# Kernel tuning notes

Hardware: AMD Instinct MI355X
Metric: run time of the kernel (lower is better)

The kernel has to match this reference:

```python
import jax, jax.numpy as jnp
import numpy as np

N_NODES = 100000
N_EDGES = 1600000
D = 128


def _graph_conv(x, src, dst, norm_src, norm_dst, W, b):
    # DGL GraphConv, norm='both': out = D_dst^{-1/2} A D_src^{-1/2} x W + b
    xs = x * norm_src[:, None]                 # [N, d] scale by src (out-)degree
    agg = jax.ops.segment_sum(xs[src], dst, num_segments=N_NODES)  # SpMM
    hd = agg * norm_dst[:, None]
    return hd @ W + b


def setup_inputs() -> dict:
    key = jax.random.key(0)
    ks = jax.random.split(key, 9)
    h = jax.random.normal(ks[0], (N_NODES, D), dtype=jnp.float32)
    src = jax.random.randint(ks[1], (N_EDGES,), 0, N_NODES, dtype=jnp.int64)
    dst = jax.random.randint(ks[2], (N_EDGES,), 0, N_NODES, dtype=jnp.int64)
    s = 1.0 / np.sqrt(D)
    W0 = jax.random.uniform(ks[3], (D, D), jnp.float32, -s, s)
    b0 = jnp.zeros((D,), jnp.float32)
    W1 = jax.random.uniform(ks[4], (D, D), jnp.float32, -s, s)
    b1 = jnp.zeros((D,), jnp.float32)
    W2 = jax.random.uniform(ks[5], (D, D), jnp.float32, -s, s)
    b2 = jnp.zeros((D,), jnp.float32)
    return {"h": h, "src": src, "dst": dst, "W0": W0, "b0": b0,
            "W1": W1, "b1": b1, "W2": W2, "b2": b2}


def reference(h, src, dst, W0, b0, W1, b1, W2, b2):
    ones = jnp.ones((N_EDGES,), jnp.float32)
    deg_out = jnp.maximum(jax.ops.segment_sum(ones, src, num_segments=N_NODES), 1.0)
    deg_in = jnp.maximum(jax.ops.segment_sum(ones, dst, num_segments=N_NODES), 1.0)
    norm_src = deg_out ** -0.5
    norm_dst = deg_in ** -0.5

    x = jax.nn.relu(_graph_conv(h, src, dst, norm_src, norm_dst, W0, b0))
    x = jax.nn.relu(_graph_conv(x, src, dst, norm_src, norm_dst, W1, b1))
    x = _graph_conv(x, src, dst, norm_src, norm_dst, W2, b2)
    # dgl.mean_nodes over a single graph -> [1, out_size]
    return jnp.mean(x, axis=0, keepdims=True)
```

## Files before the change

kernel.cpp:

```cpp
#include <hip/hip_runtime.h>
#include <hip/hip_fp16.h>

#define N_NODES 100000
#define N_EDGES 1600000
#define D 128
#define BKT_SHIFT 9
#define BKT_N 512
#define NBKT 196
#define CAP 10240
#define NBLK_B 512
#define EPB (N_EDGES / NBLK_B)
#define ZUINT4 ((2 * N_NODES + 128) / 4)

typedef _Float16 f16x4 __attribute__((ext_vector_type(4)));
typedef _Float16 f16x8 __attribute__((ext_vector_type(8)));
typedef float f32x4 __attribute__((ext_vector_type(4)));
typedef float f32x2 __attribute__((ext_vector_type(2)));

__global__ __launch_bounds__(256) void
k_zwt(const float* __restrict__ W0, const float* __restrict__ W1,
      __half* __restrict__ Wt, uint4* __restrict__ zbase,
      unsigned int* __restrict__ gcur) {
    if (blockIdx.x < 128) {
        int i = blockIdx.x * 256 + threadIdx.x;
        int l = i >> 14, r = i & (D * D - 1);
        int n = r >> 7, k = r & 127;
        const float* W = l ? W1 : W0;
        Wt[i] = __float2half(W[k * D + n]);
        return;
    }
    if (blockIdx.x == 128 && threadIdx.x < NBKT)
        gcur[threadIdx.x] = (unsigned)threadIdx.x * CAP;
    int i = (blockIdx.x - 128) * 256 + threadIdx.x;
    if (i < ZUINT4) zbase[i] = (uint4){0u, 0u, 0u, 0u};
}

__global__ __launch_bounds__(256) void
k_bucket(const int* __restrict__ src, const int* __restrict__ dst,
         unsigned int* __restrict__ gcur, unsigned int* __restrict__ packed,
         int* __restrict__ cnt_src) {
    __shared__ int hist[NBKT];
    __shared__ unsigned int base[NBKT];
    __shared__ int cur[NBKT];
    int tid = threadIdx.x;
    for (int i = tid; i < NBKT; i += 256) hist[i] = 0;
    __syncthreads();
    int e0 = blockIdx.x * EPB;
    for (int i = e0 + tid; i < e0 + EPB; i += 256)
        atomicAdd(&hist[dst[i] >> BKT_SHIFT], 1);
    __syncthreads();
    for (int i = tid; i < NBKT; i += 256) {
        base[i] = atomicAdd(&gcur[i], (unsigned)hist[i]);
        cur[i] = 0;
    }
    __syncthreads();
    for (int i = e0 + tid; i < e0 + EPB; i += 256) {
        int d = dst[i], s = src[i];
        int b = d >> BKT_SHIFT;
        int off = atomicAdd(&cur[b], 1);
        unsigned int pos = base[b] + (unsigned)off;
        if (pos < (unsigned)(b + 1) * CAP)
            packed[pos] = ((unsigned)(d & (BKT_N - 1)) << 17) | (unsigned)s;
        atomicAdd(&cnt_src[s], 1);
    }
}

__global__ __launch_bounds__(256) void
k_cscan(const unsigned int* __restrict__ gcur, int* __restrict__ cbase,
        int* __restrict__ rpD) {
    __shared__ int sc[2][256];
    int tid = threadIdx.x;
    int m = (tid < NBKT) ? (int)(gcur[tid] - (unsigned)tid * CAP) : 0;
    sc[0][tid] = m;
    int pb = 0;
    for (int d = 1; d < 256; d <<= 1) {
        __syncthreads();
        int v = sc[pb][tid];
        if (tid >= d) v += sc[pb][tid - d];
        sc[pb ^ 1][tid] = v;
        pb ^= 1;
    }
    __syncthreads();
    cbase[tid] = tid ? sc[pb][tid - 1] : 0;
    if (tid == 255) { cbase[256] = sc[pb][255]; rpD[N_NODES] = sc[pb][255]; }
}

__global__ __launch_bounds__(256) void
k_csr(const unsigned int* __restrict__ gcur, const int* __restrict__ cbase,
      const unsigned int* __restrict__ packed, int* __restrict__ csr_src,
      int* __restrict__ rpD, float* __restrict__ nd) {
    __shared__ int cnt[BKT_N];
    __shared__ int sc[2][BKT_N];
    __shared__ int outb[CAP];
    int tid = threadIdx.x;
    int b = blockIdx.x;
    int m = (int)(gcur[b] - (unsigned)b * CAP);
    if (m > CAP) m = CAP;
    int base_in = b * CAP;
    int base_out = cbase[b];
    int n0 = b * BKT_N;
    for (int j = tid; j < BKT_N; j += 256) cnt[j] = 0;
    __syncthreads();
    for (int i = tid; i < m; i += 256)
        atomicAdd(&cnt[packed[base_in + i] >> 17], 1);
    __syncthreads();
    for (int j = tid; j < BKT_N; j += 256) sc[0][j] = cnt[j];
    int pb = 0;
    for (int d = 1; d < BKT_N; d <<= 1) {
        __syncthreads();
        for (int j = tid; j < BKT_N; j += 256) {
            int v = sc[pb][j];
            if (j >= d) v += sc[pb][j - d];
            sc[pb ^ 1][j] = v;
        }
        pb ^= 1;
    }
    __syncthreads();
    for (int j = tid; j < BKT_N; j += 256) {
        int excl = j ? sc[pb][j - 1] : 0;
        int n = n0 + j;
        if (n < N_NODES) {
            rpD[n] = base_out + excl;
            nd[n] = rsqrtf((float)max(cnt[j], 1));
        }
    }
    __syncthreads();
    for (int j = tid; j < BKT_N; j += 256)
        cnt[j] = j ? sc[pb][j - 1] : 0;
    __syncthreads();
    for (int i = tid; i < m; i += 256) {
        unsigned int p = packed[base_in + i];
        int din = p >> 17;
        int off = atomicAdd(&cnt[din], 1);
        outb[off] = (int)(p & 0x1FFFFu);
    }
    __syncthreads();
    for (int i = tid; i < m; i += 256)
        csr_src[base_out + i] = outb[i];
}

__global__ void k_prep(const float* __restrict__ x, const int* __restrict__ cnt_src,
                       unsigned int* __restrict__ out) {
    int i = blockIdx.x * 256 + threadIdx.x;
    if (i >= N_NODES * (D / 4)) return;
    int n = i >> 5;
    float4 v = ((const float4*)x)[i];
    float s = rsqrtf((float)max(cnt_src[n], 1));
    int u = __builtin_amdgcn_cvt_pk_fp8_f32(v.x * s, v.y * s, 0, false);
    u = __builtin_amdgcn_cvt_pk_fp8_f32(v.z * s, v.w * s, u, true);
    out[i] = (unsigned int)u;
}

__global__ __launch_bounds__(256) void
k_spmm(const unsigned char* __restrict__ x8, const int* __restrict__ row_ptr,
       const int* __restrict__ csr_src, __half* __restrict__ agg,
       const float* __restrict__ nd, float* __restrict__ wsum) {
    int wave = (blockIdx.x * blockDim.x + threadIdx.x) >> 6;
    int lane = threadIdx.x & 63;
    int hf = lane >> 5, l32 = lane & 31;
    if (wave >= N_NODES) return;
    int beg = row_ptr[wave], end = row_ptr[wave + 1];
    float ndr = wsum ? nd[wave] : 0.0f;
    float a0 = 0.f, a1 = 0.f, a2 = 0.f, a3 = 0.f;
    int j = beg;
    for (; j + 7 < end; j += 8) {
#pragma unroll
        for (int p = 0; p < 4; p++) {
            int s0 = csr_src[j + 2 * p];
            int s1 = csr_src[j + 2 * p + 1];
            int s = hf ? s1 : s0;
            unsigned int u = *(const unsigned int*)(x8 + (size_t)s * D + 4 * l32);
            f32x2 lo = __builtin_amdgcn_cvt_pk_f32_fp8(u, false);
            f32x2 hi = __builtin_amdgcn_cvt_pk_f32_fp8(u, true);
            a0 += lo[0]; a1 += lo[1]; a2 += hi[0]; a3 += hi[1];
            if (wsum && l32 == 0) unsafeAtomicAdd(&wsum[s], ndr);
        }
    }
    for (; j + 1 < end; j += 2) {
        int s0 = csr_src[j], s1 = csr_src[j + 1];
        int s = hf ? s1 : s0;
        unsigned int u = *(const unsigned int*)(x8 + (size_t)s * D + 4 * l32);
        f32x2 lo = __builtin_amdgcn_cvt_pk_f32_fp8(u, false);
        f32x2 hi = __builtin_amdgcn_cvt_pk_f32_fp8(u, true);
        a0 += lo[0]; a1 += lo[1]; a2 += hi[0]; a3 += hi[1];
        if (wsum && l32 == 0) unsafeAtomicAdd(&wsum[s], ndr);
    }
    if (j < end && hf == 0) {
        int s = csr_src[j];
        unsigned int u = *(const unsigned int*)(x8 + (size_t)s * D + 4 * l32);
        f32x2 lo = __builtin_amdgcn_cvt_pk_f32_fp8(u, false);
        f32x2 hi = __builtin_amdgcn_cvt_pk_f32_fp8(u, true);
        a0 += lo[0]; a1 += lo[1]; a2 += hi[0]; a3 += hi[1];
        if (wsum && l32 == 0) unsafeAtomicAdd(&wsum[s], ndr);
    }
    a0 += __shfl_xor(a0, 32, 64);
    a1 += __shfl_xor(a1, 32, 64);
    a2 += __shfl_xor(a2, 32, 64);
    a3 += __shfl_xor(a3, 32, 64);
    if (hf == 0) {
        f16x4 o;
        o[0] = (_Float16)a0; o[1] = (_Float16)a1; o[2] = (_Float16)a2; o[3] = (_Float16)a3;
        ((f16x4*)(agg + (size_t)wave * D))[l32] = o;
    }
}

__global__ __launch_bounds__(256) void
k_gemm_mfma(const __half* __restrict__ A, const __half* __restrict__ Wt,
            const float* __restrict__ b, const float* __restrict__ nd,
            const int* __restrict__ cnt_src, unsigned char* __restrict__ out) {
    int w = threadIdx.x >> 6, lane = threadIdx.x & 63;
    int m = lane & 15, q = lane >> 4;
    int row0 = blockIdx.x * 128 + w * 32;

    f16x8 zf;
#pragma unroll
    for (int j = 0; j < 8; j++) zf[j] = (_Float16)0;
    f16x8 af[2][4];
#pragma unroll
    for (int g = 0; g < 2; g++) {
        int arow = row0 + g * 16 + m;
        const f16x8* pa = (const f16x8*)(A + (size_t)arow * D);
        bool aok = arow < N_NODES;
#pragma unroll
        for (int ks = 0; ks < 4; ks++) af[g][ks] = aok ? pa[ks * 4 + q] : zf;
    }

    const f16x8* pb = (const f16x8*)Wt;
    f32x4 acc[2][8];
#pragma unroll
    for (int g = 0; g < 2; g++)
#pragma unroll
        for (int nt = 0; nt < 8; nt++) acc[g][nt] = (f32x4){0.f, 0.f, 0.f, 0.f};

#pragma unroll
    for (int ks = 0; ks < 4; ks++) {
#pragma unroll
        for (int nt = 0; nt < 8; nt++) {
            f16x8 bf = pb[((nt * 16 + m) << 4) + (ks << 2) + q];
            acc[0][nt] = __builtin_amdgcn_mfma_f32_16x16x32_f16(af[0][ks], bf, acc[0][nt], 0, 0, 0);
            acc[1][nt] = __builtin_amdgcn_mfma_f32_16x16x32_f16(af[1][ks], bf, acc[1][nt], 0, 0, 0);
        }
    }

#pragma unroll
    for (int g = 0; g < 2; g++) {
        int er = row0 + g * 16 + q * 4;
        float sd[4], ss[4];
#pragma unroll
        for (int r = 0; r < 4; r++) {
            int n = er + r;
            bool ok = n < N_NODES;
            sd[r] = ok ? nd[n] : 0.0f;
            ss[r] = ok ? rsqrtf((float)max(cnt_src[n], 1)) : 0.0f;
        }
#pragma unroll
        for (int nt = 0; nt < 8; nt++) {
            int col = nt * 16 + m;
            float bc = b[col];
#pragma unroll
            for (int r = 0; r < 4; r++) {
                int n = er + r;
                if (n < N_NODES) {
                    float v = fmaxf(sd[r] * acc[g][nt][r] + bc, 0.0f) * ss[r];
                    int pk = __builtin_amdgcn_cvt_pk_fp8_f32(v, v, 0, false);
                    out[(size_t)n * D + col] = (unsigned char)(pk & 0xff);
                }
            }
        }
    }
}

__global__ __launch_bounds__(256) void
k_gemm_red(const __half* __restrict__ A, const __half* __restrict__ Wt,
           const float* __restrict__ b, const float* __restrict__ nd,
           const int* __restrict__ cnt_src, const float* __restrict__ wsum,
           float* __restrict__ colsum) {
    __shared__ float red[128];
    int tid = threadIdx.x;
    if (tid < 128) red[tid] = 0.0f;
    __syncthreads();

    int w = tid >> 6, lane = tid & 63;
    int m = lane & 15, q = lane >> 4;
    int row0 = blockIdx.x * 128 + w * 32;

    f16x8 zf;
#pragma unroll
    for (int j = 0; j < 8; j++) zf[j] = (_Float16)0;
    f16x8 af[2][4];
#pragma unroll
    for (int g = 0; g < 2; g++) {
        int arow = row0 + g * 16 + m;
        const f16x8* pa = (const f16x8*)(A + (size_t)arow * D);
        bool aok = arow < N_NODES;
#pragma unroll
        for (int ks = 0; ks < 4; ks++) af[g][ks] = aok ? pa[ks * 4 + q] : zf;
    }

    const f16x8* pb = (const f16x8*)Wt;
    f32x4 acc[2][8];
#pragma unroll
    for (int g = 0; g < 2; g++)
#pragma unroll
        for (int nt = 0; nt < 8; nt++) acc[g][nt] = (f32x4){0.f, 0.f, 0.f, 0.f};

#pragma unroll
    for (int ks = 0; ks < 4; ks++) {
#pragma unroll
        for (int nt = 0; nt < 8; nt++) {
            f16x8 bf = pb[((nt * 16 + m) << 4) + (ks << 2) + q];
            acc[0][nt] = __builtin_amdgcn_mfma_f32_16x16x32_f16(af[0][ks], bf, acc[0][nt], 0, 0, 0);
            acc[1][nt] = __builtin_amdgcn_mfma_f32_16x16x32_f16(af[1][ks], bf, acc[1][nt], 0, 0, 0);
        }
    }

    float sd[2][4], sw[2][4];
#pragma unroll
    for (int g = 0; g < 2; g++) {
        int er = row0 + g * 16 + q * 4;
#pragma unroll
        for (int r = 0; r < 4; r++) {
            int n = er + r;
            bool ok = n < N_NODES;
            sd[g][r] = ok ? nd[n] : 0.0f;
            sw[g][r] = ok ? wsum[n] * rsqrtf((float)max(cnt_src[n], 1)) : 0.0f;
        }
    }
#pragma unroll
    for (int nt = 0; nt < 8; nt++) {
        int col = nt * 16 + m;
        float bc = b[col];
        float pc = 0.0f;
#pragma unroll
        for (int g = 0; g < 2; g++)
#pragma unroll
            for (int r = 0; r < 4; r++)
                pc += sw[g][r] * fmaxf(sd[g][r] * acc[g][nt][r] + bc, 0.0f);
        atomicAdd(&red[col], pc);
    }
    __syncthreads();
    if (tid < 128) unsafeAtomicAdd(&colsum[tid], red[tid]);
}

__global__ void k_final(const float* __restrict__ colsum, const float* __restrict__ W,
                        const float* __restrict__ b, float* __restrict__ out) {
    __shared__ float m[128];
    int j = threadIdx.x;
    m[j] = colsum[j] * (1.0f / N_NODES);
    __syncthreads();
    float acc = b[j];
    for (int k = 0; k < 128; k++)
        acc = fmaf(m[k], W[(size_t)k * D + j], acc);
    out[j] = acc;
}

extern "C" void kernel_launch(void* const* d_in, const int* in_sizes, int n_in,
                              void* d_out, int out_size, void* d_ws, size_t ws_size,
                              hipStream_t stream) {
    const float* h   = (const float*)d_in[0];
    const int*   src = (const int*)d_in[1];
    const int*   dst = (const int*)d_in[2];
    const float* W0  = (const float*)d_in[3];
    const float* b0  = (const float*)d_in[4];
    const float* W1  = (const float*)d_in[5];
    const float* b1  = (const float*)d_in[6];
    const float* W2  = (const float*)d_in[7];
    const float* b2  = (const float*)d_in[8];
    float* out = (float*)d_out;

    int*           cnt_src = (int*)d_ws;
    float*         wsum    = (float*)(cnt_src + N_NODES);
    float*         colsum  = wsum + N_NODES;
    float*         nd      = colsum + 128;
    int*           rpD     = (int*)(nd + N_NODES);
    unsigned int*  gcur    = (unsigned int*)(rpD + N_NODES + 4);
    int*           cbase   = (int*)(gcur + 256);
    __half*        Wt16    = (__half*)(cbase + 260);
    int*           csr_src = (int*)(Wt16 + 2 * D * D);
    unsigned int*  packed  = (unsigned int*)(csr_src + N_EDGES);
    unsigned char* x8      = (unsigned char*)packed;
    __half*        agg16   = (__half*)(x8 + (size_t)N_NODES * D);

    k_zwt<<<128 + (ZUINT4 + 255) / 256, 256, 0, stream>>>(
        W0, W1, Wt16, (uint4*)d_ws, gcur);
    k_bucket<<<NBLK_B, 256, 0, stream>>>(src, dst, gcur, packed, cnt_src);
    k_cscan<<<1, 256, 0, stream>>>(gcur, cbase, rpD);
    k_csr<<<NBKT, 256, 0, stream>>>(gcur, cbase, packed, csr_src, rpD, nd);

    k_prep<<<(N_NODES * (D / 4) + 255) / 256, 256, 0, stream>>>(h, cnt_src,
                                                                (unsigned int*)x8);

    k_spmm<<<(N_NODES + 3) / 4, 256, 0, stream>>>(x8, rpD, csr_src, agg16,
                                                  nd, (float*)nullptr);
    k_gemm_mfma<<<(N_NODES + 127) / 128, 256, 0, stream>>>(agg16, Wt16, b0, nd,
                                                           cnt_src, x8);
    k_spmm<<<(N_NODES + 3) / 4, 256, 0, stream>>>(x8, rpD, csr_src, agg16,
                                                  nd, wsum);
    k_gemm_red<<<(N_NODES + 127) / 128, 256, 0, stream>>>(agg16, Wt16 + (size_t)D * D,
                                                          b1, nd, cnt_src, wsum, colsum);
    k_final<<<1, 128, 0, stream>>>(colsum, W2, b2, out);
}
```

Before: 467.4 us.

## Split SpMM feature dimension into column stripes across separate blocks

```diff
diff --git a/kernel.cpp b/kernel.cpp
--- a/kernel.cpp
+++ b/kernel.cpp
@@ -11,6 +11,8 @@
 #define NBLK_B 512
 #define EPB (N_EDGES / NBLK_B)
 #define ZUINT4 ((2 * N_NODES + 128) / 4)
+#define NSTRIPE 4
+#define NBW ((N_NODES + 3) / 4)
 
 typedef _Float16 f16x4 __attribute__((ext_vector_type(4)));
 typedef _Float16 f16x8 __attribute__((ext_vector_type(8)));
@@ -155,52 +157,39 @@
 k_spmm(const unsigned char* __restrict__ x8, const int* __restrict__ row_ptr,
        const int* __restrict__ csr_src, __half* __restrict__ agg,
        const float* __restrict__ nd, float* __restrict__ wsum) {
-    int wave = (blockIdx.x * blockDim.x + threadIdx.x) >> 6;
+    int stripe = blockIdx.x / NBW;
+    int bin = blockIdx.x % NBW;
+    int wave = bin * 4 + (threadIdx.x >> 6);
     int lane = threadIdx.x & 63;
-    int hf = lane >> 5, l32 = lane & 31;
     if (wave >= N_NODES) return;
+    int eo = lane >> 3;
+    int c4 = lane & 7;
     int beg = row_ptr[wave], end = row_ptr[wave + 1];
-    float ndr = wsum ? nd[wave] : 0.0f;
+    const unsigned char* xs = x8 + stripe * 32 + 4 * c4;
+    bool do_w = (wsum != nullptr) && (stripe == 0);
+    float ndr = do_w ? nd[wave] : 0.0f;
     float a0 = 0.f, a1 = 0.f, a2 = 0.f, a3 = 0.f;
-    int j = beg;
-    for (; j + 7 < end; j += 8) {
-#pragma unroll
-        for (int p = 0; p < 4; p++) {
-            int s0 = csr_src[j + 2 * p];
-            int s1 = csr_src[j + 2 * p + 1];
-            int s = hf ? s1 : s0;
-            unsigned int u = *(const unsigned int*)(x8 + (size_t)s * D + 4 * l32);
+    for (int j = beg; j < end; j += 8) {
+        int idx = j + eo;
+        if (idx < end) {
+            int s = csr_src[idx];
+            unsigned int u = *(const unsigned int*)(xs + (size_t)s * D);
             f32x2 lo = __builtin_amdgcn_cvt_pk_f32_fp8(u, false);
             f32x2 hi = __builtin_amdgcn_cvt_pk_f32_fp8(u, true);
             a0 += lo[0]; a1 += lo[1]; a2 += hi[0]; a3 += hi[1];
-            if (wsum && l32 == 0) unsafeAtomicAdd(&wsum[s], ndr);
-        }
-    }
-    for (; j + 1 < end; j += 2) {
-        int s0 = csr_src[j], s1 = csr_src[j + 1];
-        int s = hf ? s1 : s0;
-        unsigned int u = *(const unsigned int*)(x8 + (size_t)s * D + 4 * l32);
-        f32x2 lo = __builtin_amdgcn_cvt_pk_f32_fp8(u, false);
-        f32x2 hi = __builtin_amdgcn_cvt_pk_f32_fp8(u, true);
-        a0 += lo[0]; a1 += lo[1]; a2 += hi[0]; a3 += hi[1];
-        if (wsum && l32 == 0) unsafeAtomicAdd(&wsum[s], ndr);
-    }
-    if (j < end && hf == 0) {
-        int s = csr_src[j];
-        unsigned int u = *(const unsigned int*)(x8 + (size_t)s * D + 4 * l32);
-        f32x2 lo = __builtin_amdgcn_cvt_pk_f32_fp8(u, false);
-        f32x2 hi = __builtin_amdgcn_cvt_pk_f32_fp8(u, true);
-        a0 += lo[0]; a1 += lo[1]; a2 += hi[0]; a3 += hi[1];
-        if (wsum && l32 == 0) unsafeAtomicAdd(&wsum[s], ndr);
-    }
-    a0 += __shfl_xor(a0, 32, 64);
-    a1 += __shfl_xor(a1, 32, 64);
-    a2 += __shfl_xor(a2, 32, 64);
-    a3 += __shfl_xor(a3, 32, 64);
-    if (hf == 0) {
+            if (do_w && c4 == 0) unsafeAtomicAdd(&wsum[s], ndr);
+        }
+    }
+    a0 += __shfl_xor(a0, 8, 64);  a1 += __shfl_xor(a1, 8, 64);
+    a2 += __shfl_xor(a2, 8, 64);  a3 += __shfl_xor(a3, 8, 64);
+    a0 += __shfl_xor(a0, 16, 64); a1 += __shfl_xor(a1, 16, 64);
+    a2 += __shfl_xor(a2, 16, 64); a3 += __shfl_xor(a3, 16, 64);
+    a0 += __shfl_xor(a0, 32, 64); a1 += __shfl_xor(a1, 32, 64);
+    a2 += __shfl_xor(a2, 32, 64); a3 += __shfl_xor(a3, 32, 64);
+    if (eo == 0) {
         f16x4 o;
         o[0] = (_Float16)a0; o[1] = (_Float16)a1; o[2] = (_Float16)a2; o[3] = (_Float16)a3;
-        ((f16x4*)(agg + (size_t)wave * D))[l32] = o;
+        ((f16x4*)(agg + (size_t)wave * D + stripe * 32))[c4] = o;
     }
 }
 
@@ -390,12 +379,12 @@
     k_prep<<<(N_NODES * (D / 4) + 255) / 256, 256, 0, stream>>>(h, cnt_src,
                                                                 (unsigned int*)x8);
 
-    k_spmm<<<(N_NODES + 3) / 4, 256, 0, stream>>>(x8, rpD, csr_src, agg16,
-                                                  nd, (float*)nullptr);
+    k_spmm<<<NSTRIPE * NBW, 256, 0, stream>>>(x8, rpD, csr_src, agg16,
+                                              nd, (float*)nullptr);
     k_gemm_mfma<<<(N_NODES + 127) / 128, 256, 0, stream>>>(agg16, Wt16, b0, nd,
                                                            cnt_src, x8);
-    k_spmm<<<(N_NODES + 3) / 4, 256, 0, stream>>>(x8, rpD, csr_src, agg16,
-                                                  nd, wsum);
+    k_spmm<<<NSTRIPE * NBW, 256, 0, stream>>>(x8, rpD, csr_src, agg16,
+                                              nd, wsum);
     k_gemm_red<<<(N_NODES + 127) / 128, 256, 0, stream>>>(agg16, Wt16 + (size_t)D * D,
                                                           b1, nd, cnt_src, wsum, colsum);
     k_final<<<1, 128, 0, stream>>>(colsum, W2, b2, out);
```

After: 637.6 us. 1.36x slower.

## Register-cache edges in bucketing and scatter CSR directly with 512-thread blocks

Applied to the files above, without the earlier changes.

```diff
diff --git a/kernel.cpp b/kernel.cpp
--- a/kernel.cpp
+++ b/kernel.cpp
@@ -8,8 +8,9 @@
 #define BKT_N 512
 #define NBKT 196
 #define CAP 10240
-#define NBLK_B 512
-#define EPB (N_EDGES / NBLK_B)
+#define NBLK_B 625
+#define EPT 10
+#define EPB (256 * EPT)
 #define ZUINT4 ((2 * N_NODES + 128) / 4)
 
 typedef _Float16 f16x4 __attribute__((ext_vector_type(4)));
@@ -45,23 +46,30 @@
     int tid = threadIdx.x;
     for (int i = tid; i < NBKT; i += 256) hist[i] = 0;
     __syncthreads();
-    int e0 = blockIdx.x * EPB;
-    for (int i = e0 + tid; i < e0 + EPB; i += 256)
-        atomicAdd(&hist[dst[i] >> BKT_SHIFT], 1);
+    int e0 = blockIdx.x * EPB + tid;
+    int dloc[EPT], sloc[EPT];
+#pragma unroll
+    for (int k = 0; k < EPT; k++) {
+        int d = dst[e0 + k * 256];
+        int s = src[e0 + k * 256];
+        dloc[k] = d; sloc[k] = s;
+        atomicAdd(&hist[d >> BKT_SHIFT], 1);
+        atomicAdd(&cnt_src[s], 1);
+    }
     __syncthreads();
     for (int i = tid; i < NBKT; i += 256) {
         base[i] = atomicAdd(&gcur[i], (unsigned)hist[i]);
         cur[i] = 0;
     }
     __syncthreads();
-    for (int i = e0 + tid; i < e0 + EPB; i += 256) {
-        int d = dst[i], s = src[i];
+#pragma unroll
+    for (int k = 0; k < EPT; k++) {
+        int d = dloc[k], s = sloc[k];
         int b = d >> BKT_SHIFT;
         int off = atomicAdd(&cur[b], 1);
         unsigned int pos = base[b] + (unsigned)off;
         if (pos < (unsigned)(b + 1) * CAP)
             packed[pos] = ((unsigned)(d & (BKT_N - 1)) << 17) | (unsigned)s;
-        atomicAdd(&cnt_src[s], 1);
     }
 }
 
@@ -85,13 +93,13 @@
     if (tid == 255) { cbase[256] = sc[pb][255]; rpD[N_NODES] = sc[pb][255]; }
 }
 
-__global__ __launch_bounds__(256) void
+__global__ __launch_bounds__(512) void
 k_csr(const unsigned int* __restrict__ gcur, const int* __restrict__ cbase,
       const unsigned int* __restrict__ packed, int* __restrict__ csr_src,
       int* __restrict__ rpD, float* __restrict__ nd) {
     __shared__ int cnt[BKT_N];
     __shared__ int sc[2][BKT_N];
-    __shared__ int outb[CAP];
+    __shared__ int cur[BKT_N];
     int tid = threadIdx.x;
     int b = blockIdx.x;
     int m = (int)(gcur[b] - (unsigned)b * CAP);
@@ -99,44 +107,36 @@
     int base_in = b * CAP;
     int base_out = cbase[b];
     int n0 = b * BKT_N;
-    for (int j = tid; j < BKT_N; j += 256) cnt[j] = 0;
-    __syncthreads();
-    for (int i = tid; i < m; i += 256)
+    cnt[tid] = 0;
+    __syncthreads();
+    for (int i = tid; i < m; i += 512)
         atomicAdd(&cnt[packed[base_in + i] >> 17], 1);
     __syncthreads();
-    for (int j = tid; j < BKT_N; j += 256) sc[0][j] = cnt[j];
+    int v = cnt[tid];
+    sc[0][tid] = v;
     int pb = 0;
     for (int d = 1; d < BKT_N; d <<= 1) {
         __syncthreads();
-        for (int j = tid; j < BKT_N; j += 256) {
-            int v = sc[pb][j];
-            if (j >= d) v += sc[pb][j - d];
-            sc[pb ^ 1][j] = v;
-        }
+        int t = sc[pb][tid];
+        if (tid >= d) t += sc[pb][tid - d];
+        sc[pb ^ 1][tid] = t;
         pb ^= 1;
     }
     __syncthreads();
-    for (int j = tid; j < BKT_N; j += 256) {
-        int excl = j ? sc[pb][j - 1] : 0;
-        int n = n0 + j;
-        if (n < N_NODES) {
-            rpD[n] = base_out + excl;
-            nd[n] = rsqrtf((float)max(cnt[j], 1));
-        }
-    }
-    __syncthreads();
-    for (int j = tid; j < BKT_N; j += 256)
-        cnt[j] = j ? sc[pb][j - 1] : 0;
-    __syncthreads();
-    for (int i = tid; i < m; i += 256) {
+    int excl = sc[pb][tid] - v;
+    int n = n0 + tid;
+    if (n < N_NODES) {
+        rpD[n] = base_out + excl;
+        nd[n] = rsqrtf((float)max(v, 1));
+    }
+    cur[tid] = excl;
+    __syncthreads();
+    for (int i = tid; i < m; i += 512) {
         unsigned int p = packed[base_in + i];
         int din = p >> 17;
-        int off = atomicAdd(&cnt[din], 1);
-        outb[off] = (int)(p & 0x1FFFFu);
-    }
-    __syncthreads();
-    for (int i = tid; i < m; i += 256)
-        csr_src[base_out + i] = outb[i];
+        int off = atomicAdd(&cur[din], 1);
+        csr_src[base_out + off] = (int)(p & 0x1FFFFu);
+    }
 }
 
 __global__ void k_prep(const float* __restrict__ x, const int* __restrict__ cnt_src,
@@ -385,7 +385,7 @@
         W0, W1, Wt16, (uint4*)d_ws, gcur);
     k_bucket<<<NBLK_B, 256, 0, stream>>>(src, dst, gcur, packed, cnt_src);
     k_cscan<<<1, 256, 0, stream>>>(gcur, cbase, rpD);
-    k_csr<<<NBKT, 256, 0, stream>>>(gcur, cbase, packed, csr_src, rpD, nd);
+    k_csr<<<NBKT, 512, 0, stream>>>(gcur, cbase, packed, csr_src, rpD, nd);
 
     k_prep<<<(N_NODES * (D / 4) + 255) / 256, 256, 0, stream>>>(h, cnt_src,
                                                                 (unsigned int*)x8);
```

After: 467.8 us. No clear change (+0.1%).
